# Kernel optimization log

Hardware: AMD Instinct MI355X
Metric: run time of the kernel (lower is better)

## Reference

```python
import jax, jax.numpy as jnp
import numpy as np

N_NODES = 100_000
N_EDGES = 3_200_000


def setup_inputs() -> dict:
    key = jax.random.key(0)
    ks = jax.random.split(key, 8)
    x = jax.random.normal(ks[0], (N_NODES, 16), dtype=jnp.float32)
    edge_index = jax.random.randint(ks[1], (2, N_EDGES), 0, N_NODES, dtype=jnp.int64)
    edge_attr = jax.random.normal(ks[2], (N_EDGES, 8), dtype=jnp.float32)
    # lin1: Linear(8, 16); conv nn: Linear(16, 32)
    lin1_w = jax.random.normal(ks[3], (16, 8), dtype=jnp.float32) / np.sqrt(8.0)
    lin1_b = jax.random.normal(ks[4], (16,), dtype=jnp.float32) * 0.01
    nn_w = jax.random.normal(ks[5], (32, 16), dtype=jnp.float32) / np.sqrt(16.0)
    nn_b = jax.random.normal(ks[6], (32,), dtype=jnp.float32) * 0.01
    return {"x": x, "edge_index": edge_index, "edge_attr": edge_attr,
            "lin1_w": lin1_w, "lin1_b": lin1_b, "nn_w": nn_w, "nn_b": nn_b}


def reference(x, edge_index, edge_attr, lin1_w, lin1_b, nn_w, nn_b):
    # edge embedding: lin1(edge_attr)  [E, 16]
    edge_emb = edge_attr @ lin1_w.T + lin1_b
    src, dst = edge_index[0], edge_index[1]  # PyG: x_j = x[src], aggregate at dst
    # GINE message: ReLU(x_j + e_ij)
    msg = jax.nn.relu(x[src] + edge_emb)  # [E, 16]
    # sum aggregation per destination node
    aggr = jax.ops.segment_sum(msg, dst, num_segments=x.shape[0])  # [N, 16]
    # update: nn((1 + eps) * x + aggr), eps = 0
    out = (x + aggr) @ nn_w.T + nn_b  # [N, 32]
    return out
```

## Files before the change

kernel.cpp:

```cpp
#include <hip/hip_runtime.h>

#define N_NODES 100000
#define N_EDGES 3200000
#define RCHUNK  2048
#define NCHUNK  49
#define NSEG    (N_EDGES / 16)
#define BLK_E   1024
#define WQ_CAP  320
#define BLK_N   512
#define SMAX    10

__global__ __launch_bounds__(256) void gine_pack(
    const int* __restrict__ ei, unsigned char* __restrict__ cid8,
    int* __restrict__ pk)
{
    const int i = blockIdx.x * 256 + threadIdx.x;
    if (i >= N_EDGES / 4) return;
    const int4 s4 = reinterpret_cast<const int4*>(ei)[i];
    const int4 d4 = reinterpret_cast<const int4*>(ei + N_EDGES)[i];
    const unsigned cw = (unsigned)(d4.x >> 11)
                      | ((unsigned)(d4.y >> 11) << 8)
                      | ((unsigned)(d4.z >> 11) << 16)
                      | ((unsigned)(d4.w >> 11) << 24);
    reinterpret_cast<unsigned*>(cid8)[i] = cw;
    int4 p;
    p.x = s4.x | ((d4.x & (RCHUNK - 1)) << 17);
    p.y = s4.y | ((d4.y & (RCHUNK - 1)) << 17);
    p.z = s4.z | ((d4.z & (RCHUNK - 1)) << 17);
    p.w = s4.w | ((d4.w & (RCHUNK - 1)) << 17);
    reinterpret_cast<int4*>(pk)[i] = p;
}

__global__ __launch_bounds__(BLK_E, 4) void gine_edge(
    const float* __restrict__ x,
    const float* __restrict__ ea,
    const unsigned char* __restrict__ cid8,
    const int*   __restrict__ pk,
    const float* __restrict__ w1,
    const float* __restrict__ b1,
    float*       __restrict__ partial,
    int S)
{
    __shared__ float acc[16 * RCHUNK];
    __shared__ int   wq[16][WQ_CAP];
    __shared__ float s_w[128];
    __shared__ float s_b[16];

    const int t    = threadIdx.x;
    const int lane = t & 63;
    const int wid  = t >> 6;
    const int cid  = blockIdx.x % NCHUNK;
    const int sid  = blockIdx.x / NCHUNK;

    for (int i = t; i < 16 * RCHUNK / 4; i += BLK_E)
        reinterpret_cast<float4*>(acc)[i] = make_float4(0.f, 0.f, 0.f, 0.f);
    if (t < 128) s_w[t] = w1[t];
    if (t < 16)  s_b[t] = b1[t];
    __syncthreads();

    auto body = [&](int e) {
        const int pe  = pk[e];
        const int src = pe & 0x1FFFF;
        const int dl  = pe >> 17;
        const float4* eap = reinterpret_cast<const float4*>(ea) + (size_t)e * 2;
        const float4 a0 = eap[0];
        const float4 a1 = eap[1];
        const float av[8] = {a0.x,a0.y,a0.z,a0.w, a1.x,a1.y,a1.z,a1.w};
        const float4* xp = reinterpret_cast<const float4*>(x) + (size_t)src * 4;
        const float4 x0 = xp[0], x1 = xp[1], x2 = xp[2], x3 = xp[3];
        const float xv[16] = {x0.x,x0.y,x0.z,x0.w, x1.x,x1.y,x1.z,x1.w,
                              x2.x,x2.y,x2.z,x2.w, x3.x,x3.y,x3.z,x3.w};
        #pragma unroll
        for (int j = 0; j < 16; ++j) {
            float v = s_b[j];
            #pragma unroll
            for (int k = 0; k < 8; ++k)
                v = fmaf(av[k], s_w[j * 8 + k], v);
            v = fmaxf(v + xv[j], 0.0f);
            __hip_atomic_fetch_add(&acc[j * RCHUNK + dl], v,
                                   __ATOMIC_RELAXED, __HIP_MEMORY_SCOPE_WORKGROUP);
        }
    };

    const long long s0 = (long long)NSEG * sid / S;
    const long long s1 = (long long)NSEG * (sid + 1) / S;
    const unsigned long long ltmask = (1ull << lane) - 1ull;
    int cnt = 0;

    for (long long sb = s0; sb < s1; sb += BLK_E) {
        const long long seg = sb + t;
        uint4 cw = make_uint4(~0u, ~0u, ~0u, ~0u);
        if (seg < s1) cw = reinterpret_cast<const uint4*>(cid8)[seg];
        const int ebase = (int)(seg << 4);
        const unsigned w4[4] = {cw.x, cw.y, cw.z, cw.w};
        #pragma unroll
        for (int g = 0; g < 4; ++g) {
            #pragma unroll
            for (int kk = 0; kk < 4; ++kk) {
                const int k = g * 4 + kk;
                const unsigned c = (w4[g] >> (8 * kk)) & 255u;
                const bool m = (c == (unsigned)cid);
                const unsigned long long mask = __ballot(m);
                if (m) wq[wid][cnt + __popcll(mask & ltmask)] = ebase + k;
                cnt += __popcll(mask);
            }
            while (cnt >= 64) {
                body(wq[wid][cnt - 64 + lane]);
                cnt -= 64;
            }
        }
    }
    while (cnt > 0) {
        const int take = cnt < 64 ? cnt : 64;
        if (lane < take) body(wq[wid][cnt - take + lane]);
        cnt -= take;
    }

    __syncthreads();
    float4* pp = reinterpret_cast<float4*>(partial) +
                 (size_t)(sid * NCHUNK + cid) * (16 * RCHUNK / 4);
    const float4* a4 = reinterpret_cast<const float4*>(acc);
    for (int i = t; i < 16 * RCHUNK / 4; i += BLK_E)
        pp[i] = a4[i];
}

__global__ __launch_bounds__(BLK_N) void gine_node(
    const float* __restrict__ x,
    const float* __restrict__ partial,
    const float* __restrict__ w2,
    const float* __restrict__ b2,
    float*       __restrict__ out,
    int S)
{
    __shared__ float s_w[512];
    __shared__ float s_b[32];
    const int t = threadIdx.x;
    s_w[t] = w2[t];
    if (t < 32) s_b[t] = b2[t];
    __syncthreads();

    const int n = blockIdx.x * BLK_N + t;
    if (n >= N_NODES) return;
    const int c = n >> 11;
    const int l = n & (RCHUNK - 1);

    float h[16];
    const float4* xp = reinterpret_cast<const float4*>(x) + (size_t)n * 4;
    #pragma unroll
    for (int i = 0; i < 4; ++i) {
        const float4 xv = xp[i];
        h[4*i+0] = xv.x; h[4*i+1] = xv.y; h[4*i+2] = xv.z; h[4*i+3] = xv.w;
    }
    for (int s = 0; s < S; ++s) {
        const float* pb = partial + (size_t)(s * NCHUNK + c) * (16 * RCHUNK);
        #pragma unroll
        for (int j = 0; j < 16; ++j)
            h[j] += pb[j * RCHUNK + l];
    }

    float4* op = reinterpret_cast<float4*>(out) + (size_t)n * 8;
    #pragma unroll
    for (int jq = 0; jq < 8; ++jq) {
        float4 o;
        float* po = &o.x;
        #pragma unroll
        for (int jj = 0; jj < 4; ++jj) {
            const int j = jq * 4 + jj;
            float v = s_b[j];
            #pragma unroll
            for (int k = 0; k < 16; ++k)
                v = fmaf(h[k], s_w[j * 16 + k], v);
            po[jj] = v;
        }
        op[jq] = o;
    }
}

extern "C" void kernel_launch(void* const* d_in, const int* in_sizes, int n_in,
                              void* d_out, int out_size, void* d_ws, size_t ws_size,
                              hipStream_t stream) {
    const float* x  = (const float*)d_in[0];
    const int*   ei = (const int*)  d_in[1];
    const float* ea = (const float*)d_in[2];
    const float* w1 = (const float*)d_in[3];
    const float* b1 = (const float*)d_in[4];
    const float* w2 = (const float*)d_in[5];
    const float* b2 = (const float*)d_in[6];
    float* out = (float*)d_out;

    unsigned char* cid8 = (unsigned char*)d_ws;
    int*   pk      = (int*)((char*)d_ws + 3200000);
    float* partial = (float*)((char*)d_ws + 16000000);
    const long long perSlice = (long long)NCHUNK * 16 * RCHUNK * 4;
    long long avail = (long long)ws_size - 16000000LL;
    int S = (int)(avail / perSlice);
    if (S > SMAX) S = SMAX;
    if (S < 1) S = 1;

    gine_pack<<<N_EDGES / 4 / 256, 256, 0, stream>>>(ei, cid8, pk);
    gine_edge<<<NCHUNK * S, BLK_E, 0, stream>>>(x, ea, cid8, pk, w1, b1, partial, S);
    gine_node<<<(N_NODES + BLK_N - 1) / BLK_N, BLK_N, 0, stream>>>(
        x, partial, w2, b2, out, S);
}
```

Measured before the change: 827.6 us.

## Halve node chunk size and batch four edges per lane in gather drain

Halves the destination chunk to 1024 nodes, which doubles the chunk count. It drops the block to 512 threads and caps the slice count at 5, so the LDS accumulator is 64KB and two blocks can share a CU. The drain now waits for 256 queued edges and has each lane gather 4 edges' indices, edge attributes and source features up front before computing and doing LDS atomics. The aim is to raise memory-level parallelism for the random gathers. In exchange, each cid8 byte stream is scanned by many more blocks, and register pressure rises with the batched loads.

```diff
diff --git a/kernel.cpp b/kernel.cpp
--- a/kernel.cpp
+++ b/kernel.cpp
@@ -2,13 +2,14 @@
 
 #define N_NODES 100000
 #define N_EDGES 3200000
-#define RCHUNK  2048
-#define NCHUNK  49
+#define RCHUNK  1024
+#define NCHUNK  98
 #define NSEG    (N_EDGES / 16)
-#define BLK_E   1024
-#define WQ_CAP  320
+#define BLK_E   512
+#define NWAVE   (BLK_E / 64)
+#define WQ_CAP  384
 #define BLK_N   512
-#define SMAX    10
+#define SMAX    5
 
 __global__ __launch_bounds__(256) void gine_pack(
     const int* __restrict__ ei, unsigned char* __restrict__ cid8,
@@ -18,10 +19,10 @@
     if (i >= N_EDGES / 4) return;
     const int4 s4 = reinterpret_cast<const int4*>(ei)[i];
     const int4 d4 = reinterpret_cast<const int4*>(ei + N_EDGES)[i];
-    const unsigned cw = (unsigned)(d4.x >> 11)
-                      | ((unsigned)(d4.y >> 11) << 8)
-                      | ((unsigned)(d4.z >> 11) << 16)
-                      | ((unsigned)(d4.w >> 11) << 24);
+    const unsigned cw = (unsigned)(d4.x >> 10)
+                      | ((unsigned)(d4.y >> 10) << 8)
+                      | ((unsigned)(d4.z >> 10) << 16)
+                      | ((unsigned)(d4.w >> 10) << 24);
     reinterpret_cast<unsigned*>(cid8)[i] = cw;
     int4 p;
     p.x = s4.x | ((d4.x & (RCHUNK - 1)) << 17);
@@ -42,7 +43,7 @@
     int S)
 {
     __shared__ float acc[16 * RCHUNK];
-    __shared__ int   wq[16][WQ_CAP];
+    __shared__ int   wq[NWAVE][WQ_CAP];
     __shared__ float s_w[128];
     __shared__ float s_b[16];
 
@@ -82,6 +83,53 @@
         }
     };
 
+    auto drain4 = [&](int qb) {
+        int e[4], p[4];
+        #pragma unroll
+        for (int i = 0; i < 4; ++i) e[i] = wq[wid][qb + i * 64 + lane];
+        #pragma unroll
+        for (int i = 0; i < 4; ++i) p[i] = pk[e[i]];
+        float4 a0[4], a1[4];
+        #pragma unroll
+        for (int i = 0; i < 4; ++i) {
+            const float4* eap = reinterpret_cast<const float4*>(ea) + (size_t)e[i] * 2;
+            a0[i] = eap[0]; a1[i] = eap[1];
+        }
+        float4 xr[4][4];
+        #pragma unroll
+        for (int i = 0; i < 4; ++i) {
+            const float4* xp = reinterpret_cast<const float4*>(x)
+                             + (size_t)(p[i] & 0x1FFFF) * 4;
+            #pragma unroll
+            for (int q = 0; q < 4; ++q) xr[i][q] = xp[q];
+        }
+        #pragma unroll
+        for (int i = 0; i < 4; ++i) {
+            const int dl = p[i] >> 17;
+            const float av[8] = {a0[i].x,a0[i].y,a0[i].z,a0[i].w,
+                                 a1[i].x,a1[i].y,a1[i].z,a1[i].w};
+            float v[16];
+            #pragma unroll
+            for (int j = 0; j < 16; ++j) {
+                float s = s_b[j];
+                #pragma unroll
+                for (int k = 0; k < 8; ++k)
+                    s = fmaf(av[k], s_w[j * 8 + k], s);
+                v[j] = s;
+            }
+            const float xv[16] = {xr[i][0].x,xr[i][0].y,xr[i][0].z,xr[i][0].w,
+                                  xr[i][1].x,xr[i][1].y,xr[i][1].z,xr[i][1].w,
+                                  xr[i][2].x,xr[i][2].y,xr[i][2].z,xr[i][2].w,
+                                  xr[i][3].x,xr[i][3].y,xr[i][3].z,xr[i][3].w};
+            #pragma unroll
+            for (int j = 0; j < 16; ++j) {
+                const float r = fmaxf(v[j] + xv[j], 0.0f);
+                __hip_atomic_fetch_add(&acc[j * RCHUNK + dl], r,
+                                       __ATOMIC_RELAXED, __HIP_MEMORY_SCOPE_WORKGROUP);
+            }
+        }
+    };
+
     const long long s0 = (long long)NSEG * sid / S;
     const long long s1 = (long long)NSEG * (sid + 1) / S;
     const unsigned long long ltmask = (1ull << lane) - 1ull;
@@ -94,26 +142,29 @@
         const int ebase = (int)(seg << 4);
         const unsigned w4[4] = {cw.x, cw.y, cw.z, cw.w};
         #pragma unroll
-        for (int g = 0; g < 4; ++g) {
-            #pragma unroll
-            for (int kk = 0; kk < 4; ++kk) {
-                const int k = g * 4 + kk;
-                const unsigned c = (w4[g] >> (8 * kk)) & 255u;
-                const bool m = (c == (unsigned)cid);
-                const unsigned long long mask = __ballot(m);
-                if (m) wq[wid][cnt + __popcll(mask & ltmask)] = ebase + k;
-                cnt += __popcll(mask);
+        for (int w = 0; w < 4; ++w) {
+            #pragma unroll
+            for (int h = 0; h < 2; ++h) {
+                #pragma unroll
+                for (int kk = 0; kk < 2; ++kk) {
+                    const int b = h * 2 + kk;
+                    const unsigned c = (w4[w] >> (8 * b)) & 255u;
+                    const bool m = (c == (unsigned)cid);
+                    const unsigned long long mask = __ballot(m);
+                    if (m) wq[wid][cnt + __popcll(mask & ltmask)] = ebase + w * 4 + b;
+                    cnt += __popcll(mask);
+                }
+                while (cnt >= 256) { drain4(cnt - 256); cnt -= 256; }
             }
-            while (cnt >= 64) {
-                body(wq[wid][cnt - 64 + lane]);
-                cnt -= 64;
-            }
-        }
-    }
-    while (cnt > 0) {
-        const int take = cnt < 64 ? cnt : 64;
-        if (lane < take) body(wq[wid][cnt - take + lane]);
-        cnt -= take;
+        }
+    }
+    while (cnt >= 64) {
+        #pragma unroll 1
+        for (int z = 0; z < 1; ++z) body(wq[wid][cnt - 64 + lane]);
+        cnt -= 64;
+    }
+    if (cnt > 0) {
+        if (lane < cnt) body(wq[wid][lane]);
     }
 
     __syncthreads();
@@ -141,7 +192,7 @@
 
     const int n = blockIdx.x * BLK_N + t;
     if (n >= N_NODES) return;
-    const int c = n >> 11;
+    const int c = n >> 10;
     const int l = n & (RCHUNK - 1);
 
     float h[16];
@@ -192,10 +243,8 @@
     int*   pk      = (int*)((char*)d_ws + 3200000);
     float* partial = (float*)((char*)d_ws + 16000000);
     const long long perSlice = (long long)NCHUNK * 16 * RCHUNK * 4;
-    long long avail = (long long)ws_size - 16000000LL;
-    int S = (int)(avail / perSlice);
-    if (S > SMAX) S = SMAX;
-    if (S < 1) S = 1;
+    int S = SMAX;
+    while (S > 1 && 16000000LL + (long long)S * perSlice > (long long)ws_size) --S;
 
     gine_pack<<<N_EDGES / 4 / 256, 256, 0, stream>>>(ei, cid8, pk);
     gine_edge<<<NCHUNK * S, BLK_E, 0, stream>>>(x, ea, cid8, pk, w1, b1, partial, S);
```

Measured after the change: 725.0 us. 1.14x faster.
